# Optimization experiments

Measured on AMD Instinct MI355X. Metric: run time of the kernel, lower is better.

The kernel has to match this reference:

```python
import jax, jax.numpy as jnp
import numpy as np


def setup_inputs() -> dict:
    key = jax.random.key(0)
    ks = jax.random.split(key, 6)
    N, Tx, Ty = 8, 1024, 128
    enc_dim, dec_dim, Ca = 512, 1024, 128
    sc = 0.02
    return {
        "h": jax.random.normal(ks[0], (N, Tx, enc_dim), jnp.float32),
        "s": jax.random.normal(ks[1], (N, Ty, dec_dim), jnp.float32),
        "Wh": jax.random.normal(ks[2], (enc_dim, Ca), jnp.float32) * sc,
        "Ws": jax.random.normal(ks[3], (dec_dim, Ca), jnp.float32) * sc,
        "b": jax.random.normal(ks[4], (Ca,), jnp.float32) * sc,
        "v": jax.random.normal(ks[5], (Ca,), jnp.float32) * sc,
    }


def reference(h, s, Wh, Ws, b, v):
    # W([h;s]) + b == h@Wh + s@Ws + b (split of the concat Linear weight)
    ph = jnp.einsum("nxc,ca->nxa", h, Wh)            # (N, Tx, Ca)
    ps = jnp.einsum("nyd,da->nya", s, Ws) + b        # (N, Ty, Ca)
    # broadcast-add -> tanh -> dot with v : (N, Ty, Tx)
    e = jnp.einsum("nyxa,a->nyx", jnp.tanh(ps[:, :, None, :] + ph[:, None, :, :]), v)
    return jax.nn.softmax(e, axis=-1)                # attention over Tx
```

## Files before the change

### kernel.cpp

```cpp
#include <hip/hip_runtime.h>
#include <stdint.h>


typedef float  f32x4  __attribute__((ext_vector_type(4)));
typedef __bf16 bf16x8 __attribute__((ext_vector_type(8)));

#define LOG2E     1.4426950408889634f
#define TWO_LOG2E 2.8853900817779268f

__global__ void __launch_bounds__(256) transpose_cast(
    const float* __restrict__ Wh, const float* __restrict__ Ws,
    __bf16* __restrict__ WhT, __bf16* __restrict__ WsT)
{
    int bid = blockIdx.x;
    const float* src; __bf16* dst; int K, c0;
    if (bid < 8) { src = Wh; dst = WhT; K = 512;  c0 = bid * 64; }
    else         { src = Ws; dst = WsT; K = 1024; c0 = (bid - 8) * 64; }
    __shared__ float tile[64][129];
    int t = threadIdx.x;
    for (int i = 0; i < 8192; i += 256) {
        int idx = i + t;
        int r = idx >> 7, col = idx & 127;
        tile[r][col] = src[(size_t)(c0 + r) * 128 + col];
    }
    __syncthreads();
    for (int i = 0; i < 8192; i += 256) {
        int idx = i + t;
        int a = idx >> 6, cc = idx & 63;
        dst[(size_t)a * K + c0 + cc] = (__bf16)tile[cc][a];
    }
}

__global__ void __launch_bounds__(256) gemm_fused(
    const __bf16* __restrict__ WhT, const __bf16* __restrict__ WsT,
    const float* __restrict__ h, const float* __restrict__ s,
    float* __restrict__ Eph, float* __restrict__ Eps,
    const float* __restrict__ bias)
{
    int bid = blockIdx.x;
    int tid = threadIdx.x, lane = tid & 63, w = tid >> 6;
    int mbase = (w & 1) * 64;
    const __bf16* A; const float* B; float* Cp; int K; bool isPs;
    int colg;
    if (bid < 256) {
        isPs = false; A = WhT; B = h; K = 512;
        colg = bid * 32 + (w >> 1) * 16;
        int n = colg >> 10, x = colg & 1023;
        Cp = Eph + (size_t)n * 131072 + x;
    } else {
        isPs = true; A = WsT; B = s; K = 1024;
        colg = (bid - 256) * 32 + (w >> 1) * 16;
        Cp = Eps + colg;
    }
    int q = lane >> 4;
    const float*  Bp = B + (size_t)(colg + (lane & 15)) * K + q * 8;
    const __bf16* Ap = A + (size_t)(mbase + (lane & 15)) * K + q * 8;

    f32x4 acc[4] = {};
    float4 b0 = *(const float4*)(Bp);
    float4 b1 = *(const float4*)(Bp + 4);
    bf16x8 a_[4];
    #pragma unroll
    for (int i = 0; i < 4; ++i) a_[i] = *(const bf16x8*)(Ap + (size_t)i * 16 * K);

    for (int k0 = 0; k0 < K; k0 += 32) {
        int kn = k0 + 32; if (kn > K - 32) kn = K - 32;
        float4 nb0 = *(const float4*)(Bp + kn);
        float4 nb1 = *(const float4*)(Bp + kn + 4);
        bf16x8 na[4];
        #pragma unroll
        for (int i = 0; i < 4; ++i)
            na[i] = *(const bf16x8*)(Ap + (size_t)i * 16 * K + kn);
        bf16x8 bf;
        bf[0] = (__bf16)b0.x; bf[1] = (__bf16)b0.y;
        bf[2] = (__bf16)b0.z; bf[3] = (__bf16)b0.w;
        bf[4] = (__bf16)b1.x; bf[5] = (__bf16)b1.y;
        bf[6] = (__bf16)b1.z; bf[7] = (__bf16)b1.w;
        #pragma unroll
        for (int i = 0; i < 4; ++i)
            acc[i] = __builtin_amdgcn_mfma_f32_16x16x32_bf16(a_[i], bf, acc[i], 0, 0, 0);
        b0 = nb0; b1 = nb1;
        #pragma unroll
        for (int i = 0; i < 4; ++i) a_[i] = na[i];
    }

    int col = lane & 15;
    #pragma unroll
    for (int i = 0; i < 4; ++i) {
        #pragma unroll
        for (int r = 0; r < 4; ++r) {
            int m = mbase + i * 16 + q * 4 + r;
            float vv = acc[i][r];
            if (isPs) vv += bias[m];
            Cp[(size_t)m * 1024 + col] =
                __builtin_amdgcn_exp2f(vv * TWO_LOG2E);
        }
    }
}

__global__ void __launch_bounds__(512, 4) attn_softmax(
    const float* __restrict__ Eph, const float* __restrict__ Eps,
    const float* __restrict__ v, float* __restrict__ out)
{
    int bid = blockIdx.x;
    int n = bid >> 6, yg = bid & 63;
    int ny = n * 128 + yg * 2;
    const float2* ph2 = (const float2*)(Eph + (size_t)n * 131072);
    int t = threadIdx.x;

    __shared__ float4 pv_s[128];
    __shared__ float wred[2][8];
    __shared__ float VsumS;

    if (t < 128) {
        float2 p = *(const float2*)(Eps + (size_t)t * 1024 + ny);
        float4 pk; pk.x = p.x; pk.y = p.y; pk.z = v[t]; pk.w = 0.f;
        pv_s[t] = pk;
    }
    if (t < 64) {
        float vv = v[t] + v[t + 64];
        for (int m = 32; m; m >>= 1) vv += __shfl_xor(vv, m);
        if (t == 0) VsumS = vv;
    }
    __syncthreads();
    float Vsum = VsumS;

    float acc00 = 0.f, acc01 = 0.f, acc10 = 0.f, acc11 = 0.f;
    #pragma unroll 8
    for (int a = 0; a < 128; ++a) {
        float4 pq = pv_s[a];
        float2 p2 = ph2[a * 512 + t];
        float z00 = fmaf(pq.x, p2.x, 1.f);
        float z01 = fmaf(pq.x, p2.y, 1.f);
        float z10 = fmaf(pq.y, p2.x, 1.f);
        float z11 = fmaf(pq.y, p2.y, 1.f);
        acc00 = fmaf(pq.z, __builtin_amdgcn_rcpf(z00), acc00);
        acc01 = fmaf(pq.z, __builtin_amdgcn_rcpf(z01), acc01);
        acc10 = fmaf(pq.z, __builtin_amdgcn_rcpf(z10), acc10);
        acc11 = fmaf(pq.z, __builtin_amdgcn_rcpf(z11), acc11);
    }
    float e00 = fmaf(-2.f, acc00, Vsum);
    float e01 = fmaf(-2.f, acc01, Vsum);
    float e10 = fmaf(-2.f, acc10, Vsum);
    float e11 = fmaf(-2.f, acc11, Vsum);

    int lane = t & 63, wv = t >> 6;
    float mx0 = fmaxf(e00, e01), mx1 = fmaxf(e10, e11);
    for (int m = 32; m; m >>= 1) {
        mx0 = fmaxf(mx0, __shfl_xor(mx0, m));
        mx1 = fmaxf(mx1, __shfl_xor(mx1, m));
    }
    if (lane == 0) { wred[0][wv] = mx0; wred[1][wv] = mx1; }
    __syncthreads();
    mx0 = wred[0][0]; mx1 = wred[1][0];
    #pragma unroll
    for (int i = 1; i < 8; ++i) {
        mx0 = fmaxf(mx0, wred[0][i]);
        mx1 = fmaxf(mx1, wred[1][i]);
    }
    __syncthreads();
    float s00 = __builtin_amdgcn_exp2f((e00 - mx0) * LOG2E);
    float s01 = __builtin_amdgcn_exp2f((e01 - mx0) * LOG2E);
    float s10 = __builtin_amdgcn_exp2f((e10 - mx1) * LOG2E);
    float s11 = __builtin_amdgcn_exp2f((e11 - mx1) * LOG2E);
    float sm0 = s00 + s01, sm1 = s10 + s11;
    for (int m = 32; m; m >>= 1) {
        sm0 += __shfl_xor(sm0, m);
        sm1 += __shfl_xor(sm1, m);
    }
    if (lane == 0) { wred[0][wv] = sm0; wred[1][wv] = sm1; }
    __syncthreads();
    sm0 = 0.f; sm1 = 0.f;
    #pragma unroll
    for (int i = 0; i < 8; ++i) { sm0 += wred[0][i]; sm1 += wred[1][i]; }
    float r0 = __builtin_amdgcn_rcpf(sm0);
    float r1 = __builtin_amdgcn_rcpf(sm1);
    float2 o0; o0.x = s00 * r0; o0.y = s01 * r0;
    float2 o1; o1.x = s10 * r1; o1.y = s11 * r1;
    ((float2*)(out + (size_t)(ny + 0) * 1024))[t] = o0;
    ((float2*)(out + (size_t)(ny + 1) * 1024))[t] = o1;
}

extern "C" void kernel_launch(void* const* d_in, const int* in_sizes, int n_in,
                              void* d_out, int out_size, void* d_ws, size_t ws_size,
                              hipStream_t stream) {
    const float* h  = (const float*)d_in[0];
    const float* s  = (const float*)d_in[1];
    const float* Wh = (const float*)d_in[2];
    const float* Ws = (const float*)d_in[3];
    const float* b  = (const float*)d_in[4];
    const float* v  = (const float*)d_in[5];
    float* out = (float*)d_out;

    char* ws = (char*)d_ws;
    float*  Eph = (float*)ws;
    float*  Eps = (float*)(ws + (4u << 20));
    __bf16* WhT = (__bf16*)(ws + (4u << 20) + (512u << 10));
    __bf16* WsT = WhT + (size_t)128 * 512;

    transpose_cast<<<24, 256, 0, stream>>>(Wh, Ws, WhT, WsT);
    gemm_fused<<<288, 256, 0, stream>>>(WhT, WsT, h, s, Eph, Eps, b);
    attn_softmax<<<512, 512, 0, stream>>>(Eph, Eps, v, out);
}
```

Baseline: 132.0 us.

## Process four decoder rows per attention block to reuse encoder projections

Each softmax block now computes four y rows instead of two, halving the grid and reusing each loaded ph pair across four rows. This cuts L2/global reads of the encoder projection tensor per output. In exchange each CU holds fewer waves, and register pressure rises (the occupancy hint was dropped), which may reduce latency hiding.

```diff
diff --git a/kernel.cpp b/kernel.cpp
--- a/kernel.cpp
+++ b/kernel.cpp
@@ -98,87 +98,95 @@
     }
 }
 
-__global__ void __launch_bounds__(512, 4) attn_softmax(
+__global__ void __launch_bounds__(512) attn_softmax(
     const float* __restrict__ Eph, const float* __restrict__ Eps,
     const float* __restrict__ v, float* __restrict__ out)
 {
     int bid = blockIdx.x;
-    int n = bid >> 6, yg = bid & 63;
-    int ny = n * 128 + yg * 2;
+    int n = bid >> 5, yg = bid & 31;
+    int ny = n * 128 + yg * 4;
     const float2* ph2 = (const float2*)(Eph + (size_t)n * 131072);
     int t = threadIdx.x;
 
-    __shared__ float4 pv_s[128];
-    __shared__ float wred[2][8];
-    __shared__ float VsumS;
+    __shared__ float4 ps_s[128];
+    __shared__ float  v_s[128];
+    __shared__ float  wred[4][8];
+    __shared__ float  VsumS;
 
     if (t < 128) {
-        float2 p = *(const float2*)(Eps + (size_t)t * 1024 + ny);
-        float4 pk; pk.x = p.x; pk.y = p.y; pk.z = v[t]; pk.w = 0.f;
-        pv_s[t] = pk;
-    }
-    if (t < 64) {
-        float vv = v[t] + v[t + 64];
+        ps_s[t] = *(const float4*)(Eps + (size_t)t * 1024 + ny);
+        v_s[t]  = v[t];
+    } else if (t < 192) {
+        int l = t - 128;
+        float vv = v[l] + v[l + 64];
         for (int m = 32; m; m >>= 1) vv += __shfl_xor(vv, m);
-        if (t == 0) VsumS = vv;
+        if (l == 0) VsumS = vv;
     }
     __syncthreads();
     float Vsum = VsumS;
 
-    float acc00 = 0.f, acc01 = 0.f, acc10 = 0.f, acc11 = 0.f;
-    #pragma unroll 8
+    float acc0[4] = {0, 0, 0, 0}, acc1[4] = {0, 0, 0, 0};
+    #pragma unroll 4
     for (int a = 0; a < 128; ++a) {
-        float4 pq = pv_s[a];
-        float2 p2 = ph2[a * 512 + t];
-        float z00 = fmaf(pq.x, p2.x, 1.f);
-        float z01 = fmaf(pq.x, p2.y, 1.f);
-        float z10 = fmaf(pq.y, p2.x, 1.f);
-        float z11 = fmaf(pq.y, p2.y, 1.f);
-        acc00 = fmaf(pq.z, __builtin_amdgcn_rcpf(z00), acc00);
-        acc01 = fmaf(pq.z, __builtin_amdgcn_rcpf(z01), acc01);
-        acc10 = fmaf(pq.z, __builtin_amdgcn_rcpf(z10), acc10);
-        acc11 = fmaf(pq.z, __builtin_amdgcn_rcpf(z11), acc11);
-    }
-    float e00 = fmaf(-2.f, acc00, Vsum);
-    float e01 = fmaf(-2.f, acc01, Vsum);
-    float e10 = fmaf(-2.f, acc10, Vsum);
-    float e11 = fmaf(-2.f, acc11, Vsum);
+        float4 ps4 = ps_s[a];
+        float  va  = v_s[a];
+        float2 p2  = ph2[a * 512 + t];
+        float psy[4] = {ps4.x, ps4.y, ps4.z, ps4.w};
+        #pragma unroll
+        for (int y = 0; y < 4; ++y) {
+            float z0 = fmaf(psy[y], p2.x, 1.f);
+            float z1 = fmaf(psy[y], p2.y, 1.f);
+            acc0[y] = fmaf(va, __builtin_amdgcn_rcpf(z0), acc0[y]);
+            acc1[y] = fmaf(va, __builtin_amdgcn_rcpf(z1), acc1[y]);
+        }
+    }
+
+    float e0[4], e1[4];
+    #pragma unroll
+    for (int y = 0; y < 4; ++y) {
+        e0[y] = fmaf(-2.f, acc0[y], Vsum);
+        e1[y] = fmaf(-2.f, acc1[y], Vsum);
+    }
 
     int lane = t & 63, wv = t >> 6;
-    float mx0 = fmaxf(e00, e01), mx1 = fmaxf(e10, e11);
-    for (int m = 32; m; m >>= 1) {
-        mx0 = fmaxf(mx0, __shfl_xor(mx0, m));
-        mx1 = fmaxf(mx1, __shfl_xor(mx1, m));
-    }
-    if (lane == 0) { wred[0][wv] = mx0; wred[1][wv] = mx1; }
-    __syncthreads();
-    mx0 = wred[0][0]; mx1 = wred[1][0];
-    #pragma unroll
-    for (int i = 1; i < 8; ++i) {
-        mx0 = fmaxf(mx0, wred[0][i]);
-        mx1 = fmaxf(mx1, wred[1][i]);
-    }
-    __syncthreads();
-    float s00 = __builtin_amdgcn_exp2f((e00 - mx0) * LOG2E);
-    float s01 = __builtin_amdgcn_exp2f((e01 - mx0) * LOG2E);
-    float s10 = __builtin_amdgcn_exp2f((e10 - mx1) * LOG2E);
-    float s11 = __builtin_amdgcn_exp2f((e11 - mx1) * LOG2E);
-    float sm0 = s00 + s01, sm1 = s10 + s11;
-    for (int m = 32; m; m >>= 1) {
-        sm0 += __shfl_xor(sm0, m);
-        sm1 += __shfl_xor(sm1, m);
-    }
-    if (lane == 0) { wred[0][wv] = sm0; wred[1][wv] = sm1; }
-    __syncthreads();
-    sm0 = 0.f; sm1 = 0.f;
-    #pragma unroll
-    for (int i = 0; i < 8; ++i) { sm0 += wred[0][i]; sm1 += wred[1][i]; }
-    float r0 = __builtin_amdgcn_rcpf(sm0);
-    float r1 = __builtin_amdgcn_rcpf(sm1);
-    float2 o0; o0.x = s00 * r0; o0.y = s01 * r0;
-    float2 o1; o1.x = s10 * r1; o1.y = s11 * r1;
-    ((float2*)(out + (size_t)(ny + 0) * 1024))[t] = o0;
-    ((float2*)(out + (size_t)(ny + 1) * 1024))[t] = o1;
+    #pragma unroll
+    for (int y = 0; y < 4; ++y) {
+        float mx = fmaxf(e0[y], e1[y]);
+        for (int m = 32; m; m >>= 1) mx = fmaxf(mx, __shfl_xor(mx, m));
+        if (lane == 0) wred[y][wv] = mx;
+    }
+    __syncthreads();
+    float mxv[4];
+    #pragma unroll
+    for (int y = 0; y < 4; ++y) {
+        float mx = wred[y][0];
+        #pragma unroll
+        for (int i = 1; i < 8; ++i) mx = fmaxf(mx, wred[y][i]);
+        mxv[y] = mx;
+    }
+    __syncthreads();
+    float s0[4], s1[4], smv[4];
+    #pragma unroll
+    for (int y = 0; y < 4; ++y) {
+        s0[y] = __builtin_amdgcn_exp2f((e0[y] - mxv[y]) * LOG2E);
+        s1[y] = __builtin_amdgcn_exp2f((e1[y] - mxv[y]) * LOG2E);
+        float sm = s0[y] + s1[y];
+        for (int m = 32; m; m >>= 1) sm += __shfl_xor(sm, m);
+        if (lane == 0) wred[y][wv] = sm;
+    }
+    __syncthreads();
+    #pragma unroll
+    for (int y = 0; y < 4; ++y) {
+        float sm = 0.f;
+        #pragma unroll
+        for (int i = 0; i < 8; ++i) sm += wred[y][i];
+        smv[y] = __builtin_amdgcn_rcpf(sm);
+    }
+    #pragma unroll
+    for (int y = 0; y < 4; ++y) {
+        float2 o; o.x = s0[y] * smv[y]; o.y = s1[y] * smv[y];
+        ((float2*)(out + (size_t)(ny + y) * 1024))[t] = o;
+    }
 }
 
 extern "C" void kernel_launch(void* const* d_in, const int* in_sizes, int n_in,
@@ -200,5 +208,5 @@
 
     transpose_cast<<<24, 256, 0, stream>>>(Wh, Ws, WhT, WsT);
     gemm_fused<<<288, 256, 0, stream>>>(WhT, WsT, h, s, Eph, Eps, b);
-    attn_softmax<<<512, 512, 0, stream>>>(Eph, Eps, v, out);
-}
+    attn_softmax<<<256, 512, 0, stream>>>(Eph, Eps, v, out);
+}
```

Result: no change. 134.1 us (+1.6%).
